# Kernel tuning notes

Hardware: AMD Instinct MI355X
Metric: run time of the kernel (lower is better)

## Reference

```python
import jax, jax.numpy as jnp
import numpy as np

N_STEPS = 8  # fixed-step RK4 over t in [0, 1]


def setup_inputs() -> dict:
    key = jax.random.key(0)
    ks = jax.random.split(key, 4)
    B, D, H = 512, 64, 512
    x = jax.random.normal(ks[0], (B, D), jnp.float32)
    # MLP vector field f(t, x): input = concat([x, t]) -> H -> H -> D
    W1 = jax.random.normal(ks[1], (D + 1, H), jnp.float32) / jnp.sqrt(D + 1.0)
    b1 = jnp.zeros((H,), jnp.float32)
    W2 = jax.random.normal(ks[2], (H, H), jnp.float32) / jnp.sqrt(float(H))
    b2 = jnp.zeros((H,), jnp.float32)
    W3 = jax.random.normal(ks[3], (H, D), jnp.float32) / jnp.sqrt(float(H))
    b3 = jnp.zeros((D,), jnp.float32)
    return {"x": x, "W1": W1, "b1": b1, "W2": W2, "b2": b2, "W3": W3, "b3": b3}


def reference(x, W1, b1, W2, b2, W3, b3):
    dt = 1.0 / N_STEPS

    def vf_single(t, xi):
        # xi: [D], t: scalar -> [D]
        h = jnp.concatenate([xi, t[None]])
        h = jnp.tanh(h @ W1 + b1)
        h = jnp.tanh(h @ W2 + b2)
        return h @ W3 + b3

    def aug_dyn(t, xb):
        # dx/dt = f(x, t);  d(log_det)/dt = -trace(df/dx)  (exact divergence)
        f_s = lambda xi: vf_single(t, xi)
        dx = jax.vmap(f_s)(xb)                      # [B, D]
        jac = jax.vmap(jax.jacfwd(f_s))(xb)         # [B, D, D]
        tr = jnp.trace(jac, axis1=-2, axis2=-1)     # [B]
        return dx, -tr

    def step(carry, i):
        xb, ld = carry
        t0 = i.astype(jnp.float32) * dt
        k1x, k1l = aug_dyn(t0, xb)
        k2x, k2l = aug_dyn(t0 + 0.5 * dt, xb + 0.5 * dt * k1x)
        k3x, k3l = aug_dyn(t0 + 0.5 * dt, xb + 0.5 * dt * k2x)
        k4x, k4l = aug_dyn(t0 + dt, xb + dt * k3x)
        xb = xb + (dt / 6.0) * (k1x + 2.0 * k2x + 2.0 * k3x + k4x)
        ld = ld + (dt / 6.0) * (k1l + 2.0 * k2l + 2.0 * k3l + k4l)
        return (xb, ld), None

    ld0 = jnp.zeros((x.shape[0],), x.dtype)
    (z, log_det), _ = jax.lax.scan(step, (x, ld0), jnp.arange(N_STEPS))
    return z, log_det
```

## Files before the change

kernel.cpp:

```cpp
#include <hip/hip_runtime.h>

#define NSTEPS 8
#define DT (1.0f / NSTEPS)

typedef __bf16 bfv8 __attribute__((ext_vector_type(8)));
typedef float f32x4 __attribute__((ext_vector_type(4)));

static __device__ __forceinline__ float fast_tanh(float x) {
  float e = __expf(2.f * x);
  return 1.f - 2.f * __builtin_amdgcn_rcpf(e + 1.f);
}

static __device__ __forceinline__ f32x4 splat4(float v) {
  f32x4 r; r[0] = v; r[1] = v; r[2] = v; r[3] = v; return r;
}

__global__ __launch_bounds__(256) void pre_kernel(
    const float* __restrict__ W1, const float* __restrict__ W2,
    const float* __restrict__ W3, __bf16* __restrict__ W1P,
    __bf16* __restrict__ W2P, __bf16* __restrict__ GtP,
    __bf16* __restrict__ W3P) {
  int t = blockIdx.x * 256 + threadIdx.x;
  if (t < 4096) {
    int kq = t >> 9, col = t & 511;
    bfv8 o;
#pragma unroll
    for (int e = 0; e < 8; ++e) o[e] = (__bf16)W1[(kq * 8 + e) * 512 + col];
    *(bfv8*)(W1P + t * 8) = o;
  } else if (t < 36864) {
    int g = t - 4096;
    int kc = g >> 9, col = g & 511;
    bfv8 o;
#pragma unroll
    for (int e = 0; e < 8; ++e) o[e] = (__bf16)W2[(kc * 8 + e) * 512 + col];
    *(bfv8*)(W2P + g * 8) = o;
  } else if (t < 69632) {
    int g = t - 36864;
    int kc = g >> 9, j = g & 511;
    float w1c[64];
#pragma unroll
    for (int m = 0; m < 64; ++m) w1c[m] = W1[m * 512 + j];
    bfv8 o;
#pragma unroll
    for (int e = 0; e < 8; ++e) {
      int k = kc * 8 + e;
      float s = 0.f;
#pragma unroll
      for (int m = 0; m < 64; ++m) s = fmaf(w1c[m], W3[k * 64 + m], s);
      o[e] = (__bf16)(s * W2[j * 512 + k]);
    }
    *(bfv8*)(GtP + g * 8) = o;
  } else if (t < 73728) {
    int g = t - 69632;
    int kc = g >> 6, m = g & 63;
    bfv8 o;
#pragma unroll
    for (int e = 0; e < 8; ++e) o[e] = (__bf16)W3[(kc * 8 + e) * 64 + m];
    *(bfv8*)(W3P + g * 8) = o;
  }
}

__global__ __launch_bounds__(512, 2) void cnf_kernel(
    const float* __restrict__ x, const float* __restrict__ b1,
    const float* __restrict__ W1, const float* __restrict__ b2,
    const float* __restrict__ b3, const __bf16* __restrict__ W1P,
    const __bf16* __restrict__ W2P, const __bf16* __restrict__ GtP,
    const __bf16* __restrict__ W3P, float* __restrict__ out) {
  __shared__ __bf16 h1s[8192];
  __shared__ __bf16 h2s[8192];
  __shared__ __bf16 vs[8192];
  __shared__ __bf16 xins[1024];
  __shared__ float kcur[1024];
  __shared__ float trbuf[16];

  const int tid = threadIdx.x;
  const int lane = tid & 63;
  const int w = tid >> 6;
  const int lr = lane & 15;
  const int lq = lane >> 4;
  const int rowbase = blockIdx.x * 16;
  const char* h1c = (const char*)h1s;
  const char* h2c = (const char*)h2s;
  const char* vsc = (const char*)vs;

  float b1c[4], w1tc[4], b2c[4], b3c[4];
#pragma unroll
  for (int n = 0; n < 4; ++n) {
    const int col = (w * 4 + n) * 16 + lr;
    b1c[n] = b1[col];
    w1tc[n] = W1[64 * 512 + col];
    b2c[n] = b2[col];
    b3c[n] = b3[n * 16 + lr];
  }

  float xbA = 0.f, xbB = 0.f, kaA = 0.f, kaB = 0.f, ldv = 0.f, ldacc = 0.f;

#pragma unroll 1
  for (int ev = 0; ev <= 4 * NSTEPS; ++ev) {
    const int g = ev & 3;
    {
      float xwA, xwB;
      if (ev == 0) {
        xbA = x[rowbase * 64 + tid];
        xbB = x[rowbase * 64 + 512 + tid];
        xwA = xbA; xwB = xbB;
        kcur[tid] = 0.f; kcur[tid + 512] = 0.f;
        if (tid < 16) trbuf[tid] = 0.f;
      } else {
        const int gp = (ev - 1) & 3;
        const float k0 = kcur[tid], k1 = kcur[tid + 512];
        kcur[tid] = 0.f; kcur[tid + 512] = 0.f;
        float tv = 0.f;
        if (tid < 16) { tv = trbuf[tid]; trbuf[tid] = 0.f; }
        if (gp < 3) {
          const float wg = (gp == 0) ? 1.f : 2.f;
          const float cn = (gp == 2) ? DT : 0.5f * DT;
          kaA += wg * k0; kaB += wg * k1;
          xwA = xbA + cn * k0; xwB = xbB + cn * k1;
          if (tid < 16) ldacc += wg * tv;
        } else {
          xbA += (DT / 6.f) * (kaA + k0);
          xbB += (DT / 6.f) * (kaB + k1);
          kaA = 0.f; kaB = 0.f;
          xwA = xbA; xwB = xbB;
          if (tid < 16) { ldv -= (DT / 6.f) * (ldacc + tv); ldacc = 0.f; }
        }
      }
      if (ev == 4 * NSTEPS) {
        out[rowbase * 64 + tid] = xwA;
        out[rowbase * 64 + 512 + tid] = xwB;
        if (tid < 16) out[512 * 64 + rowbase + tid] = ldv;
        break;
      }
      xins[tid] = (__bf16)xwA;
      xins[tid + 512] = (__bf16)xwB;
    }
    __syncthreads();

    {
      const float tval =
          (ev >> 2) * DT + ((g == 0) ? 0.f : (g == 3) ? DT : 0.5f * DT);
      const bfv8 a0 = *(const bfv8*)&xins[lr * 64 + lq * 8];
      const bfv8 a1 = *(const bfv8*)&xins[lr * 64 + 32 + lq * 8];
      bfv8 ring[4];
#pragma unroll
      for (int p = 0; p < 4; ++p)
        ring[p] = *(const bfv8*)(W1P + ((p & 1) * 4 + lq) * 4096 +
                                 ((w * 4 + (p >> 1)) * 16 + lr) * 8);
      f32x4 C = splat4(0.f);
#pragma unroll
      for (int f = 0; f < 8; ++f) {
        const int n = f >> 1, h = f & 1;
        if (h == 0) C = splat4(b1c[n] + tval * w1tc[n]);
        C = __builtin_amdgcn_mfma_f32_16x16x32_bf16(h ? a1 : a0, ring[f & 3],
                                                    C, 0, 0, 0);
        if (f < 4) {
          const int f4 = f + 4;
          ring[f & 3] = *(const bfv8*)(W1P + ((f4 & 1) * 4 + lq) * 4096 +
                                       ((w * 4 + (f4 >> 1)) * 16 + lr) * 8);
        }
        if (h == 1) {
#pragma unroll
          for (int r = 0; r < 4; ++r) {
            const int row = lq * 4 + r;
            const int col = (w * 4 + n) * 16 + lr;
            *(__bf16*)((char*)h1s + row * 1024 +
                       ((col * 2) ^ ((row & 7) << 4))) = (__bf16)fast_tanh(C[r]);
          }
        }
      }
    }
    __syncthreads();

    {
      bfv8 A[16];
#pragma unroll
      for (int c = 0; c < 16; ++c)
        A[c] = *(const bfv8*)(h1c + lr * 1024 +
                              (((c * 64) + lq * 16) ^ ((lr & 7) << 4)));
      bfv8 ring[4];
#pragma unroll
      for (int p = 0; p < 4; ++p)
        ring[p] = *(const bfv8*)(W2P + (p * 4 + lq) * 4096 +
                                 ((w * 4) * 16 + lr) * 8);
      f32x4 C = splat4(0.f);
#pragma unroll
      for (int f = 0; f < 64; ++f) {
        const int c = f & 15, t = f >> 4;
        if (c == 0) C = splat4(0.f);
        C = __builtin_amdgcn_mfma_f32_16x16x32_bf16(A[c], ring[f & 3], C, 0, 0,
                                                    0);
        if (f < 60) {
          const int f4 = f + 4;
          ring[f & 3] = *(const bfv8*)(W2P + ((f4 & 15) * 4 + lq) * 4096 +
                                       ((w * 4 + (f4 >> 4)) * 16 + lr) * 8);
        }
        if (c == 15) {
#pragma unroll
          for (int r = 0; r < 4; ++r) {
            const int row = lq * 4 + r;
            const int col = (w * 4 + t) * 16 + lr;
            const float tv = fast_tanh(C[r] + b2c[t]);
            const int bo = row * 1024 + ((col * 2) ^ ((row & 7) << 4));
            *(__bf16*)((char*)h2s + bo) = (__bf16)tv;
            *(__bf16*)((char*)vs + bo) = (__bf16)(1.f - tv * tv);
          }
        }
      }
    }
    __syncthreads();

    {
      bfv8 A[16];
#pragma unroll
      for (int c = 0; c < 16; ++c)
        A[c] = *(const bfv8*)(vsc + lr * 1024 +
                              (((c * 64) + lq * 16) ^ ((lr & 7) << 4)));
      bfv8 ring[4];
#pragma unroll
      for (int p = 0; p < 4; ++p)
        ring[p] = *(const bfv8*)(GtP + (p * 4 + lq) * 4096 +
                                 ((w * 4) * 16 + lr) * 8);
      f32x4 C = splat4(0.f);
      float pacc[4] = {0.f, 0.f, 0.f, 0.f};
#pragma unroll
      for (int f = 0; f < 64; ++f) {
        const int c = f & 15, t = f >> 4;
        if (c == 0) C = splat4(0.f);
        C = __builtin_amdgcn_mfma_f32_16x16x32_bf16(A[c], ring[f & 3], C, 0, 0,
                                                    0);
        if (f < 60) {
          const int f4 = f + 4;
          ring[f & 3] = *(const bfv8*)(GtP + ((f4 & 15) * 4 + lq) * 4096 +
                                       ((w * 4 + (f4 >> 4)) * 16 + lr) * 8);
        }
        if (c == 15) {
#pragma unroll
          for (int r = 0; r < 4; ++r) {
            const int row = lq * 4 + r;
            const int col = (w * 4 + t) * 16 + lr;
            const float h1v = (float)*(const __bf16*)(
                h1c + row * 1024 + ((col * 2) ^ ((row & 7) << 4)));
            pacc[r] += C[r] * (1.f - h1v * h1v);
          }
        }
      }
#pragma unroll
      for (int r = 0; r < 4; ++r) {
        float p = pacc[r];
        p += __shfl_xor(p, 1);
        p += __shfl_xor(p, 2);
        p += __shfl_xor(p, 4);
        p += __shfl_xor(p, 8);
        if (lr == 0) atomicAdd(&trbuf[lq * 4 + r], p);
      }
    }

    {
      bfv8 A2[2];
#pragma unroll
      for (int h = 0; h < 2; ++h)
        A2[h] = *(const bfv8*)(h2c + lr * 1024 +
                               (((w * 128 + h * 64 + lq * 16)) ^
                                ((lr & 7) << 4)));
      bfv8 ring[4];
#pragma unroll
      for (int p = 0; p < 4; ++p)
        ring[p] = *(const bfv8*)(W3P + (w * 8 + (p & 1) * 4 + lq) * 512 +
                                 ((p >> 1) * 16 + lr) * 8);
      f32x4 C = splat4(0.f);
#pragma unroll
      for (int f = 0; f < 8; ++f) {
        const int mt = f >> 1, h = f & 1;
        if (h == 0) C = splat4((w == 0) ? b3c[mt] : 0.f);
        C = __builtin_amdgcn_mfma_f32_16x16x32_bf16(A2[h], ring[f & 3], C, 0,
                                                    0, 0);
        if (f < 4) {
          const int f4 = f + 4;
          ring[f & 3] =
              *(const bfv8*)(W3P + (w * 8 + (f4 & 1) * 4 + lq) * 512 +
                             ((f4 >> 1) * 16 + lr) * 8);
        }
        if (h == 1) {
#pragma unroll
          for (int r = 0; r < 4; ++r)
            atomicAdd(&kcur[(lq * 4 + r) * 64 + mt * 16 + lr], C[r]);
        }
      }
    }
    __syncthreads();
  }
}

extern "C" void kernel_launch(void* const* d_in, const int* in_sizes, int n_in,
                              void* d_out, int out_size, void* d_ws,
                              size_t ws_size, hipStream_t stream) {
  const float* x = (const float*)d_in[0];
  const float* W1 = (const float*)d_in[1];
  const float* b1 = (const float*)d_in[2];
  const float* W2 = (const float*)d_in[3];
  const float* b2 = (const float*)d_in[4];
  const float* W3 = (const float*)d_in[5];
  const float* b3 = (const float*)d_in[6];
  float* out = (float*)d_out;
  __bf16* wsb = (__bf16*)d_ws;

  __bf16* W1P = wsb;
  __bf16* W2P = wsb + 32768;
  __bf16* GtP = wsb + 294912;
  __bf16* W3P = wsb + 557056;

  pre_kernel<<<288, 256, 0, stream>>>(W1, W2, W3, W1P, W2P, GtP, W3P);
  cnf_kernel<<<32, 512, 0, stream>>>(x, b1, W1, b2, b3, W1P, W2P, GtP, W3P,
                                     out);
}
```

Before: 1.085 ms.

## Stream weights through triple-buffered LDS ring via async global_load_lds

```diff
diff --git a/kernel.cpp b/kernel.cpp
--- a/kernel.cpp
+++ b/kernel.cpp
@@ -1,4 +1,5 @@
 #include <hip/hip_runtime.h>
+#include <stdint.h>
 
 #define NSTEPS 8
 #define DT (1.0f / NSTEPS)
@@ -10,9 +11,36 @@
   float e = __expf(2.f * x);
   return 1.f - 2.f * __builtin_amdgcn_rcpf(e + 1.f);
 }
-
 static __device__ __forceinline__ f32x4 splat4(float v) {
   f32x4 r; r[0] = v; r[1] = v; r[2] = v; r[3] = v; return r;
+}
+
+#define FENCE __builtin_amdgcn_sched_barrier(0)
+#define PIPEBAR()                                                  \
+  do {                                                             \
+    FENCE;                                                         \
+    asm volatile("s_waitcnt vmcnt(4) lgkmcnt(0)" ::: "memory");    \
+    __builtin_amdgcn_s_barrier();                                  \
+    FENCE;                                                         \
+  } while (0)
+#define ENDBAR()                                                   \
+  do {                                                             \
+    FENCE;                                                         \
+    asm volatile("s_waitcnt lgkmcnt(0)" ::: "memory");             \
+    __builtin_amdgcn_s_barrier();                                  \
+    FENCE;                                                         \
+  } while (0)
+
+static __device__ __forceinline__ void stage_chunk(const char* gsrc,
+                                                   char* ldst, int tid) {
+#pragma unroll
+  for (int i = 0; i < 4; ++i)
+    __builtin_amdgcn_global_load_lds(
+        (const __attribute__((address_space(1))) uint32_t*)(gsrc + i * 8192 +
+                                                            tid * 16),
+        (__attribute__((address_space(3))) uint32_t*)(ldst + i * 8192 +
+                                                      tid * 16),
+        16, 0, 0);
 }
 
 __global__ __launch_bounds__(256) void pre_kernel(
@@ -63,12 +91,11 @@
 __global__ __launch_bounds__(512, 2) void cnf_kernel(
     const float* __restrict__ x, const float* __restrict__ b1,
     const float* __restrict__ W1, const float* __restrict__ b2,
-    const float* __restrict__ b3, const __bf16* __restrict__ W1P,
-    const __bf16* __restrict__ W2P, const __bf16* __restrict__ GtP,
+    const float* __restrict__ b3, const char* __restrict__ stream,
     const __bf16* __restrict__ W3P, float* __restrict__ out) {
+  __shared__ char ring[3 * 32768];
   __shared__ __bf16 h1s[8192];
   __shared__ __bf16 h2s[8192];
-  __shared__ __bf16 vs[8192];
   __shared__ __bf16 xins[1024];
   __shared__ float kcur[1024];
   __shared__ float trbuf[16];
@@ -81,7 +108,6 @@
   const int rowbase = blockIdx.x * 16;
   const char* h1c = (const char*)h1s;
   const char* h2c = (const char*)h2s;
-  const char* vsc = (const char*)vs;
 
   float b1c[4], w1tc[4], b2c[4], b3c[4];
 #pragma unroll
@@ -93,11 +119,24 @@
     b3c[n] = b3[n * 16 + lr];
   }
 
+  const int bbase = lq * 8192 + w * 1024 + lr * 16;
+
   float xbA = 0.f, xbB = 0.f, kaA = 0.f, kaB = 0.f, ldv = 0.f, ldacc = 0.f;
+
+  int sc = 0;
+  stage_chunk(stream, ring, tid);
+  stage_chunk(stream + 32768, ring + 32768, tid);
+
+#define STEP_HEAD(T_NEXT)                                                \
+  do {                                                                   \
+    PIPEBAR();                                                           \
+    int ss_ = sc + 2; if (ss_ >= 3) ss_ -= 3;                            \
+    stage_chunk(stream + (T_NEXT) * 32768, ring + ss_ * 32768, tid);     \
+  } while (0)
+#define STEP_TAIL() do { sc = (sc + 1 == 3) ? 0 : sc + 1; } while (0)
 
 #pragma unroll 1
   for (int ev = 0; ev <= 4 * NSTEPS; ++ev) {
-    const int g = ev & 3;
     {
       float xwA, xwB;
       if (ev == 0) {
@@ -135,125 +174,115 @@
       xins[tid] = (__bf16)xwA;
       xins[tid + 512] = (__bf16)xwB;
     }
-    __syncthreads();
+
+    const int g = ev & 3;
+    const float tval =
+        (ev >> 2) * DT + ((g == 0) ? 0.f : (g == 3) ? DT : 0.5f * DT);
+    f32x4 C[4];
 
     {
-      const float tval =
-          (ev >> 2) * DT + ((g == 0) ? 0.f : (g == 3) ? DT : 0.5f * DT);
+      STEP_HEAD(2);
       const bfv8 a0 = *(const bfv8*)&xins[lr * 64 + lq * 8];
+      const char* bs = ring + sc * 32768 + bbase;
+#pragma unroll
+      for (int n = 0; n < 4; ++n) {
+        C[n] = splat4(b1c[n] + tval * w1tc[n]);
+        C[n] = __builtin_amdgcn_mfma_f32_16x16x32_bf16(
+            a0, *(const bfv8*)(bs + n * 256), C[n], 0, 0, 0);
+      }
+      STEP_TAIL();
+    }
+    {
+      STEP_HEAD(3);
       const bfv8 a1 = *(const bfv8*)&xins[lr * 64 + 32 + lq * 8];
-      bfv8 ring[4];
-#pragma unroll
-      for (int p = 0; p < 4; ++p)
-        ring[p] = *(const bfv8*)(W1P + ((p & 1) * 4 + lq) * 4096 +
-                                 ((w * 4 + (p >> 1)) * 16 + lr) * 8);
-      f32x4 C = splat4(0.f);
-#pragma unroll
-      for (int f = 0; f < 8; ++f) {
-        const int n = f >> 1, h = f & 1;
-        if (h == 0) C = splat4(b1c[n] + tval * w1tc[n]);
-        C = __builtin_amdgcn_mfma_f32_16x16x32_bf16(h ? a1 : a0, ring[f & 3],
-                                                    C, 0, 0, 0);
-        if (f < 4) {
-          const int f4 = f + 4;
-          ring[f & 3] = *(const bfv8*)(W1P + ((f4 & 1) * 4 + lq) * 4096 +
-                                       ((w * 4 + (f4 >> 1)) * 16 + lr) * 8);
+      const char* bs = ring + sc * 32768 + bbase;
+#pragma unroll
+      for (int n = 0; n < 4; ++n) {
+        C[n] = __builtin_amdgcn_mfma_f32_16x16x32_bf16(
+            a1, *(const bfv8*)(bs + n * 256), C[n], 0, 0, 0);
+#pragma unroll
+        for (int r = 0; r < 4; ++r) {
+          const int row = lq * 4 + r;
+          const int col = (w * 4 + n) * 16 + lr;
+          *(__bf16*)((char*)h1s + row * 1024 + ((col * 2) ^ ((row & 7) << 4))) =
+              (__bf16)fast_tanh(C[n][r]);
         }
-        if (h == 1) {
+      }
+      STEP_TAIL();
+    }
+
+#pragma unroll
+    for (int c = 0; c < 16; ++c) {
+      STEP_HEAD(c + 4);
+      if (c == 0) {
+#pragma unroll
+        for (int n = 0; n < 4; ++n) C[n] = splat4(0.f);
+      }
+      const bfv8 A = *(const bfv8*)(h1c + lr * 1024 +
+                                    (((c * 64) + lq * 16) ^ ((lr & 7) << 4)));
+      const char* bs = ring + sc * 32768 + bbase;
+#pragma unroll
+      for (int n = 0; n < 4; ++n)
+        C[n] = __builtin_amdgcn_mfma_f32_16x16x32_bf16(
+            A, *(const bfv8*)(bs + n * 256), C[n], 0, 0, 0);
+      if (c == 15) {
+#pragma unroll
+        for (int n = 0; n < 4; ++n)
 #pragma unroll
           for (int r = 0; r < 4; ++r) {
             const int row = lq * 4 + r;
             const int col = (w * 4 + n) * 16 + lr;
-            *(__bf16*)((char*)h1s + row * 1024 +
-                       ((col * 2) ^ ((row & 7) << 4))) = (__bf16)fast_tanh(C[r]);
+            const float tv = fast_tanh(C[n][r] + b2c[n]);
+            *(__bf16*)((char*)h2s + row * 1024 +
+                       ((col * 2) ^ ((row & 7) << 4))) = (__bf16)tv;
           }
-        }
-      }
-    }
-    __syncthreads();
-
-    {
-      bfv8 A[16];
-#pragma unroll
-      for (int c = 0; c < 16; ++c)
-        A[c] = *(const bfv8*)(h1c + lr * 1024 +
-                              (((c * 64) + lq * 16) ^ ((lr & 7) << 4)));
-      bfv8 ring[4];
-#pragma unroll
-      for (int p = 0; p < 4; ++p)
-        ring[p] = *(const bfv8*)(W2P + (p * 4 + lq) * 4096 +
-                                 ((w * 4) * 16 + lr) * 8);
-      f32x4 C = splat4(0.f);
-#pragma unroll
-      for (int f = 0; f < 64; ++f) {
-        const int c = f & 15, t = f >> 4;
-        if (c == 0) C = splat4(0.f);
-        C = __builtin_amdgcn_mfma_f32_16x16x32_bf16(A[c], ring[f & 3], C, 0, 0,
-                                                    0);
-        if (f < 60) {
-          const int f4 = f + 4;
-          ring[f & 3] = *(const bfv8*)(W2P + ((f4 & 15) * 4 + lq) * 4096 +
-                                       ((w * 4 + (f4 >> 4)) * 16 + lr) * 8);
-        }
-        if (c == 15) {
+      }
+      STEP_TAIL();
+    }
+
+#pragma unroll
+    for (int c = 0; c < 16; ++c) {
+      STEP_HEAD((c < 14) ? 20 + c : c - 14);
+      if (c == 0) {
+#pragma unroll
+        for (int n = 0; n < 4; ++n) C[n] = splat4(0.f);
+      }
+      const bfv8 hv = *(const bfv8*)(h2c + lr * 1024 +
+                                     (((c * 64) + lq * 16) ^ ((lr & 7) << 4)));
+      bfv8 av;
+#pragma unroll
+      for (int e = 0; e < 8; ++e) {
+        const float tv = (float)hv[e];
+        av[e] = (__bf16)(1.f - tv * tv);
+      }
+      const char* bs = ring + sc * 32768 + bbase;
+#pragma unroll
+      for (int n = 0; n < 4; ++n)
+        C[n] = __builtin_amdgcn_mfma_f32_16x16x32_bf16(
+            av, *(const bfv8*)(bs + n * 256), C[n], 0, 0, 0);
+      if (c == 15) {
+        float pacc[4] = {0.f, 0.f, 0.f, 0.f};
+#pragma unroll
+        for (int n = 0; n < 4; ++n)
 #pragma unroll
           for (int r = 0; r < 4; ++r) {
             const int row = lq * 4 + r;
-            const int col = (w * 4 + t) * 16 + lr;
-            const float tv = fast_tanh(C[r] + b2c[t]);
-            const int bo = row * 1024 + ((col * 2) ^ ((row & 7) << 4));
-            *(__bf16*)((char*)h2s + bo) = (__bf16)tv;
-            *(__bf16*)((char*)vs + bo) = (__bf16)(1.f - tv * tv);
-          }
-        }
-      }
-    }
-    __syncthreads();
-
-    {
-      bfv8 A[16];
-#pragma unroll
-      for (int c = 0; c < 16; ++c)
-        A[c] = *(const bfv8*)(vsc + lr * 1024 +
-                              (((c * 64) + lq * 16) ^ ((lr & 7) << 4)));
-      bfv8 ring[4];
-#pragma unroll
-      for (int p = 0; p < 4; ++p)
-        ring[p] = *(const bfv8*)(GtP + (p * 4 + lq) * 4096 +
-                                 ((w * 4) * 16 + lr) * 8);
-      f32x4 C = splat4(0.f);
-      float pacc[4] = {0.f, 0.f, 0.f, 0.f};
-#pragma unroll
-      for (int f = 0; f < 64; ++f) {
-        const int c = f & 15, t = f >> 4;
-        if (c == 0) C = splat4(0.f);
-        C = __builtin_amdgcn_mfma_f32_16x16x32_bf16(A[c], ring[f & 3], C, 0, 0,
-                                                    0);
-        if (f < 60) {
-          const int f4 = f + 4;
-          ring[f & 3] = *(const bfv8*)(GtP + ((f4 & 15) * 4 + lq) * 4096 +
-                                       ((w * 4 + (f4 >> 4)) * 16 + lr) * 8);
-        }
-        if (c == 15) {
-#pragma unroll
-          for (int r = 0; r < 4; ++r) {
-            const int row = lq * 4 + r;
-            const int col = (w * 4 + t) * 16 + lr;
+            const int col = (w * 4 + n) * 16 + lr;
             const float h1v = (float)*(const __bf16*)(
                 h1c + row * 1024 + ((col * 2) ^ ((row & 7) << 4)));
-            pacc[r] += C[r] * (1.f - h1v * h1v);
+            pacc[r] += C[n][r] * (1.f - h1v * h1v);
           }
+#pragma unroll
+        for (int r = 0; r < 4; ++r) {
+          float p = pacc[r];
+          p += __shfl_xor(p, 1);
+          p += __shfl_xor(p, 2);
+          p += __shfl_xor(p, 4);
+          p += __shfl_xor(p, 8);
+          if (lr == 0) atomicAdd(&trbuf[lq * 4 + r], p);
         }
       }
-#pragma unroll
-      for (int r = 0; r < 4; ++r) {
-        float p = pacc[r];
-        p += __shfl_xor(p, 1);
-        p += __shfl_xor(p, 2);
-        p += __shfl_xor(p, 4);
-        p += __shfl_xor(p, 8);
-        if (lr == 0) atomicAdd(&trbuf[lq * 4 + r], p);
-      }
+      STEP_TAIL();
     }
 
     {
@@ -261,34 +290,24 @@
 #pragma unroll
       for (int h = 0; h < 2; ++h)
         A2[h] = *(const bfv8*)(h2c + lr * 1024 +
-                               (((w * 128 + h * 64 + lq * 16)) ^
+                               ((w * 128 + h * 64 + lq * 16) ^
                                 ((lr & 7) << 4)));
-      bfv8 ring[4];
-#pragma unroll
-      for (int p = 0; p < 4; ++p)
-        ring[p] = *(const bfv8*)(W3P + (w * 8 + (p & 1) * 4 + lq) * 512 +
-                                 ((p >> 1) * 16 + lr) * 8);
-      f32x4 C = splat4(0.f);
+      f32x4 C3;
 #pragma unroll
       for (int f = 0; f < 8; ++f) {
         const int mt = f >> 1, h = f & 1;
-        if (h == 0) C = splat4((w == 0) ? b3c[mt] : 0.f);
-        C = __builtin_amdgcn_mfma_f32_16x16x32_bf16(A2[h], ring[f & 3], C, 0,
-                                                    0, 0);
-        if (f < 4) {
-          const int f4 = f + 4;
-          ring[f & 3] =
-              *(const bfv8*)(W3P + (w * 8 + (f4 & 1) * 4 + lq) * 512 +
-                             ((f4 >> 1) * 16 + lr) * 8);
+        if (h == 0) C3 = splat4((w == 0) ? b3c[mt] : 0.f);
+        const bfv8 B = *(const bfv8*)(W3P + (w * 8 + h * 4 + lq) * 512 +
+                                      (mt * 16 + lr) * 8);
+        C3 = __builtin_amdgcn_mfma_f32_16x16x32_bf16(A2[h], B, C3, 0, 0, 0);
+        if (h == 1) {
+#pragma unroll
+          for (int r = 0; r < 4; ++r)
+            atomicAdd(&kcur[(lq * 4 + r) * 64 + mt * 16 + lr], C3[r]);
         }
-        if (h == 1) {
-#pragma unroll
-          for (int r = 0; r < 4; ++r)
-            atomicAdd(&kcur[(lq * 4 + r) * 64 + mt * 16 + lr], C[r]);
-        }
-      }
-    }
-    __syncthreads();
+      }
+    }
+    ENDBAR();
   }
 }
 
@@ -311,6 +330,6 @@
   __bf16* W3P = wsb + 557056;
 
   pre_kernel<<<288, 256, 0, stream>>>(W1, W2, W3, W1P, W2P, GtP, W3P);
-  cnf_kernel<<<32, 512, 0, stream>>>(x, b1, W1, b2, b3, W1P, W2P, GtP, W3P,
+  cnf_kernel<<<32, 512, 0, stream>>>(x, b1, W1, b2, b3, (const char*)wsb, W3P,
                                      out);
 }
```

New measurement: 1.202 ms. 1.11x slower.

## Split hidden dimension across 8 blocks per row group with LDS-resident weights and inter-block sync

Applied to the files above, without the earlier changes.

```diff
diff --git a/kernel.cpp b/kernel.cpp
--- a/kernel.cpp
+++ b/kernel.cpp
@@ -1,295 +1,312 @@
 #include <hip/hip_runtime.h>
+#include <stdint.h>
 
 #define NSTEPS 8
 #define DT (1.0f / NSTEPS)
 
 typedef __bf16 bfv8 __attribute__((ext_vector_type(8)));
+typedef __bf16 bfv4 __attribute__((ext_vector_type(4)));
 typedef float f32x4 __attribute__((ext_vector_type(4)));
 
 static __device__ __forceinline__ float fast_tanh(float x) {
   float e = __expf(2.f * x);
   return 1.f - 2.f * __builtin_amdgcn_rcpf(e + 1.f);
 }
-
 static __device__ __forceinline__ f32x4 splat4(float v) {
   f32x4 r; r[0] = v; r[1] = v; r[2] = v; r[3] = v; return r;
 }
 
 __global__ __launch_bounds__(256) void pre_kernel(
     const float* __restrict__ W1, const float* __restrict__ W2,
-    const float* __restrict__ W3, __bf16* __restrict__ W1P,
-    __bf16* __restrict__ W2P, __bf16* __restrict__ GtP,
-    __bf16* __restrict__ W3P) {
+    const float* __restrict__ W3, __bf16* __restrict__ blob,
+    unsigned int* __restrict__ syncc) {
   int t = blockIdx.x * 256 + threadIdx.x;
+  if (t < 49152) syncc[t] = 0u;
+  if (t >= 73728) return;
+  bfv8 o;
+  int di;
   if (t < 4096) {
-    int kq = t >> 9, col = t & 511;
-    bfv8 o;
-#pragma unroll
-    for (int e = 0; e < 8; ++e) o[e] = (__bf16)W1[(kq * 8 + e) * 512 + col];
-    *(bfv8*)(W1P + t * 8) = o;
+    int kq = t >> 9, colg = t & 511;
+    int s = colg >> 6, c = colg & 63;
+    int f = kq >> 2, gg = (kq & 3) ^ ((c >> 1) & 3);
+    di = s * 73728 + f * 2048 + c * 32 + gg * 8;
+#pragma unroll
+    for (int e = 0; e < 8; ++e) o[e] = (__bf16)W1[(kq * 8 + e) * 512 + colg];
   } else if (t < 36864) {
-    int g = t - 4096;
-    int kc = g >> 9, col = g & 511;
-    bfv8 o;
-#pragma unroll
-    for (int e = 0; e < 8; ++e) o[e] = (__bf16)W2[(kc * 8 + e) * 512 + col];
-    *(bfv8*)(W2P + g * 8) = o;
+    int u = t - 4096;
+    int colg = u & 511, kc = u >> 9;
+    int s = colg >> 6, c = colg & 63;
+    int f = kc >> 2, gg = (kc & 3) ^ ((c >> 1) & 3);
+    di = s * 73728 + 4096 + f * 2048 + c * 32 + gg * 8;
+#pragma unroll
+    for (int e = 0; e < 8; ++e) o[e] = (__bf16)W2[(kc * 8 + e) * 512 + colg];
   } else if (t < 69632) {
-    int g = t - 36864;
-    int kc = g >> 9, j = g & 511;
+    int u = t - 36864;
+    int jg = u & 511, kc = u >> 9;
     float w1c[64];
 #pragma unroll
-    for (int m = 0; m < 64; ++m) w1c[m] = W1[m * 512 + j];
-    bfv8 o;
+    for (int m = 0; m < 64; ++m) w1c[m] = W1[m * 512 + jg];
+    int s = jg >> 6, c = jg & 63;
+    int f = kc >> 2, gg = (kc & 3) ^ ((c >> 1) & 3);
+    di = s * 73728 + 36864 + f * 2048 + c * 32 + gg * 8;
 #pragma unroll
     for (int e = 0; e < 8; ++e) {
       int k = kc * 8 + e;
-      float s = 0.f;
-#pragma unroll
-      for (int m = 0; m < 64; ++m) s = fmaf(w1c[m], W3[k * 64 + m], s);
-      o[e] = (__bf16)(s * W2[j * 512 + k]);
-    }
-    *(bfv8*)(GtP + g * 8) = o;
-  } else if (t < 73728) {
-    int g = t - 69632;
-    int kc = g >> 6, m = g & 63;
-    bfv8 o;
+      float sm = 0.f;
+#pragma unroll
+      for (int m = 0; m < 64; ++m) sm = fmaf(w1c[m], W3[k * 64 + m], sm);
+      o[e] = (__bf16)(sm * W2[jg * 512 + k]);
+    }
+  } else {
+    int u = t - 69632;
+    int m = u & 63, kc = u >> 6;
+    int tile = m >> 4, cm = m & 15;
+    int b = tile * 2 + (kc >> 5);
+    int f = (kc >> 2) & 7, gg = (kc & 3) ^ ((cm >> 1) & 3);
+    di = b * 73728 + 69632 + f * 512 + cm * 32 + gg * 8;
 #pragma unroll
     for (int e = 0; e < 8; ++e) o[e] = (__bf16)W3[(kc * 8 + e) * 64 + m];
-    *(bfv8*)(W3P + g * 8) = o;
   }
-}
-
-__global__ __launch_bounds__(512, 2) void cnf_kernel(
+  *(bfv8*)(blob + di) = o;
+}
+
+static __device__ __forceinline__ void gsync(unsigned int* cnt, int tid) {
+  __threadfence();
+  __syncthreads();
+  if (tid == 0) {
+    __hip_atomic_fetch_add(cnt, 1u, __ATOMIC_RELEASE, __HIP_MEMORY_SCOPE_AGENT);
+    int guard = 0;
+    while (__hip_atomic_load(cnt, __ATOMIC_RELAXED, __HIP_MEMORY_SCOPE_AGENT) <
+           8u) {
+      __builtin_amdgcn_s_sleep(2);
+      if (++guard > (1 << 22)) break;
+    }
+    (void)__hip_atomic_load(cnt, __ATOMIC_ACQUIRE, __HIP_MEMORY_SCOPE_AGENT);
+  }
+  __syncthreads();
+  __threadfence();
+}
+
+__global__ __launch_bounds__(256, 1) void cnf_kernel(
     const float* __restrict__ x, const float* __restrict__ b1,
-    const float* __restrict__ W1, const float* __restrict__ b2,
-    const float* __restrict__ b3, const __bf16* __restrict__ W1P,
-    const __bf16* __restrict__ W2P, const __bf16* __restrict__ GtP,
-    const __bf16* __restrict__ W3P, float* __restrict__ out) {
-  __shared__ __bf16 h1s[8192];
-  __shared__ __bf16 h2s[8192];
-  __shared__ __bf16 vs[8192];
-  __shared__ __bf16 xins[1024];
-  __shared__ float kcur[1024];
-  __shared__ float trbuf[16];
+    const float* __restrict__ W1f, const float* __restrict__ b2,
+    const float* __restrict__ b3, const __bf16* __restrict__ blob,
+    char* __restrict__ actg, unsigned int* __restrict__ syncc,
+    float* __restrict__ out) {
+  __shared__ char wlds[147456];
+  __shared__ char actv[8192];
+  __shared__ char xins[2048];
+  __shared__ float kxl[256];
+  __shared__ float trl[16];
 
   const int tid = threadIdx.x;
   const int lane = tid & 63;
   const int w = tid >> 6;
   const int lr = lane & 15;
   const int lq = lane >> 4;
-  const int rowbase = blockIdx.x * 16;
-  const char* h1c = (const char*)h1s;
-  const char* h2c = (const char*)h2s;
-  const char* vsc = (const char*)vs;
-
-  float b1c[4], w1tc[4], b2c[4], b3c[4];
-#pragma unroll
-  for (int n = 0; n < 4; ++n) {
-    const int col = (w * 4 + n) * 16 + lr;
-    b1c[n] = b1[col];
-    w1tc[n] = W1[64 * 512 + col];
-    b2c[n] = b2[col];
-    b3c[n] = b3[n * 16 + lr];
+  const int g = blockIdx.x & 31;
+  const int b = blockIdx.x >> 5;
+  const int rowbase = g * 16;
+
+  {
+    const char* src = (const char*)blob + (size_t)b * 147456;
+#pragma unroll 1
+    for (int i = 0; i < 36; ++i) {
+      const int off = (w * 36 + i) * 1024 + lane * 16;
+      __builtin_amdgcn_global_load_lds(
+          (const __attribute__((address_space(1))) uint32_t*)(src + off),
+          (__attribute__((address_space(3))) uint32_t*)(wlds + off), 16, 0, 0);
+    }
   }
 
-  float xbA = 0.f, xbB = 0.f, kaA = 0.f, kaB = 0.f, ldv = 0.f, ldacc = 0.f;
+  const int colg = b * 64 + w * 16 + lr;
+  const float b1c = b1[colg];
+  const float w1tc = W1f[64 * 512 + colg];
+  const float b2c = b2[colg];
+  const float b3v = ((b & 1) == 0) ? b3[(b >> 1) * 16 + (tid & 15)] : 0.f;
+  const int gx = lq ^ ((lr >> 1) & 3);
+  const int bcol = (w * 16 + lr) * 64 + gx * 16;
+
+  char* gb = actg + (size_t)g * 65536;
+  __bf16* h1buf = (__bf16*)gb;
+  __bf16* h2buf = (__bf16*)(gb + 16384);
+  __bf16* vbuf = (__bf16*)(gb + 32768);
+  float* kxbuf = (float*)(gb + 49152);
+  float* trbufg = (float*)(gb + 57344);
+  unsigned int* scg = syncc + g * 96 * 16;
+
+  asm volatile("s_waitcnt vmcnt(0)" ::: "memory");
+  __syncthreads();
+
+  const int srow = tid >> 4, scol = (tid & 15) * 4;
+  float xb[4], ka[4];
+  float ldv = 0.f, ldacc = 0.f;
+
+#define MFMA(A, Boff, C)                                                      \
+  C = __builtin_amdgcn_mfma_f32_16x16x32_bf16(                                \
+      A, *(const bfv8*)(wlds + (Boff)), C, 0, 0, 0)
+#define AFRAG(c)                                                              \
+  (*(const bfv8*)(actv + lr * 512 + ((((c) * 64) + lq * 16) ^ ((lr & 7) << 4))))
+#define STAGE_ACT(SRCBUF, HF)                                                 \
+  do {                                                                        \
+    const int row_ = tid >> 4, ch_ = tid & 15;                                \
+    bfv8 d0_ = *(const bfv8*)((SRCBUF) + row_ * 512 + (HF) * 256 + ch_ * 8);  \
+    bfv8 d1_ =                                                                \
+        *(const bfv8*)((SRCBUF) + row_ * 512 + (HF) * 256 + 128 + ch_ * 8);   \
+    __syncthreads();                                                          \
+    *(bfv8*)(actv + row_ * 512 + ((ch_ * 16) ^ ((row_ & 7) << 4))) = d0_;     \
+    *(bfv8*)(actv + row_ * 512 + ((ch_ * 16 + 256) ^ ((row_ & 7) << 4))) =    \
+        d1_;                                                                  \
+    __syncthreads();                                                          \
+  } while (0)
 
 #pragma unroll 1
   for (int ev = 0; ev <= 4 * NSTEPS; ++ev) {
-    const int g = ev & 3;
-    {
-      float xwA, xwB;
-      if (ev == 0) {
-        xbA = x[rowbase * 64 + tid];
-        xbB = x[rowbase * 64 + 512 + tid];
-        xwA = xbA; xwB = xbB;
-        kcur[tid] = 0.f; kcur[tid + 512] = 0.f;
-        if (tid < 16) trbuf[tid] = 0.f;
+    float xw[4];
+    if (ev == 0) {
+      const float* xr = x + (rowbase + srow) * 64 + scol;
+#pragma unroll
+      for (int i = 0; i < 4; ++i) { xb[i] = xr[i]; ka[i] = 0.f; xw[i] = xb[i]; }
+    } else {
+      const int gp = (ev - 1) & 3;
+      const int tt = scol >> 4, cb2 = scol & 15;
+      float kv[4];
+#pragma unroll
+      for (int i = 0; i < 4; ++i)
+        kv[i] = kxbuf[(tt * 2) * 256 + srow * 16 + cb2 + i] +
+                kxbuf[(tt * 2 + 1) * 256 + srow * 16 + cb2 + i];
+      float tv = 0.f;
+      if (tid < 16) {
+#pragma unroll
+        for (int bb = 0; bb < 8; ++bb) tv += trbufg[bb * 16 + tid];
+      }
+      if (gp < 3) {
+        const float wg = (gp == 0) ? 1.f : 2.f;
+        const float cn = (gp == 2) ? DT : 0.5f * DT;
+#pragma unroll
+        for (int i = 0; i < 4; ++i) {
+          ka[i] += wg * kv[i];
+          xw[i] = xb[i] + cn * kv[i];
+        }
+        if (tid < 16) ldacc += wg * tv;
       } else {
-        const int gp = (ev - 1) & 3;
-        const float k0 = kcur[tid], k1 = kcur[tid + 512];
-        kcur[tid] = 0.f; kcur[tid + 512] = 0.f;
-        float tv = 0.f;
-        if (tid < 16) { tv = trbuf[tid]; trbuf[tid] = 0.f; }
-        if (gp < 3) {
-          const float wg = (gp == 0) ? 1.f : 2.f;
-          const float cn = (gp == 2) ? DT : 0.5f * DT;
-          kaA += wg * k0; kaB += wg * k1;
-          xwA = xbA + cn * k0; xwB = xbB + cn * k1;
-          if (tid < 16) ldacc += wg * tv;
-        } else {
-          xbA += (DT / 6.f) * (kaA + k0);
-          xbB += (DT / 6.f) * (kaB + k1);
-          kaA = 0.f; kaB = 0.f;
-          xwA = xbA; xwB = xbB;
-          if (tid < 16) { ldv -= (DT / 6.f) * (ldacc + tv); ldacc = 0.f; }
+#pragma unroll
+        for (int i = 0; i < 4; ++i) {
+          xb[i] += (DT / 6.f) * (ka[i] + kv[i]);
+          ka[i] = 0.f;
+          xw[i] = xb[i];
         }
-      }
-      if (ev == 4 * NSTEPS) {
-        out[rowbase * 64 + tid] = xwA;
-        out[rowbase * 64 + 512 + tid] = xwB;
+        if (tid < 16) { ldv -= (DT / 6.f) * (ldacc + tv); ldacc = 0.f; }
+      }
+    }
+    if (ev == 4 * NSTEPS) {
+      if (b == 0) {
+        float* orow = out + (rowbase + srow) * 64 + scol;
+#pragma unroll
+        for (int i = 0; i < 4; ++i) orow[i] = xw[i];
         if (tid < 16) out[512 * 64 + rowbase + tid] = ldv;
-        break;
-      }
-      xins[tid] = (__bf16)xwA;
-      xins[tid + 512] = (__bf16)xwB;
+      }
+      break;
+    }
+    {
+      bfv4 pk;
+#pragma unroll
+      for (int i = 0; i < 4; ++i) pk[i] = (__bf16)xw[i];
+      *(bfv4*)(xins + srow * 128 + ((scol * 2) ^ ((srow & 7) << 4))) = pk;
     }
     __syncthreads();
 
-    {
-      const float tval =
-          (ev >> 2) * DT + ((g == 0) ? 0.f : (g == 3) ? DT : 0.5f * DT);
-      const bfv8 a0 = *(const bfv8*)&xins[lr * 64 + lq * 8];
-      const bfv8 a1 = *(const bfv8*)&xins[lr * 64 + 32 + lq * 8];
-      bfv8 ring[4];
-#pragma unroll
-      for (int p = 0; p < 4; ++p)
-        ring[p] = *(const bfv8*)(W1P + ((p & 1) * 4 + lq) * 4096 +
-                                 ((w * 4 + (p >> 1)) * 16 + lr) * 8);
-      f32x4 C = splat4(0.f);
-#pragma unroll
-      for (int f = 0; f < 8; ++f) {
-        const int n = f >> 1, h = f & 1;
-        if (h == 0) C = splat4(b1c[n] + tval * w1tc[n]);
-        C = __builtin_amdgcn_mfma_f32_16x16x32_bf16(h ? a1 : a0, ring[f & 3],
-                                                    C, 0, 0, 0);
-        if (f < 4) {
-          const int f4 = f + 4;
-          ring[f & 3] = *(const bfv8*)(W1P + ((f4 & 1) * 4 + lq) * 4096 +
-                                       ((w * 4 + (f4 >> 1)) * 16 + lr) * 8);
+    const int gq = ev & 3;
+    const float tval =
+        (ev >> 2) * DT + ((gq == 0) ? 0.f : (gq == 3) ? DT : 0.5f * DT);
+    float ureg[4];
+    {
+      bfv8 a0 = *(const bfv8*)(xins + lr * 128 + ((lq * 16) ^ ((lr & 7) << 4)));
+      bfv8 a1 =
+          *(const bfv8*)(xins + lr * 128 + ((64 + lq * 16) ^ ((lr & 7) << 4)));
+      f32x4 C = splat4(b1c + tval * w1tc);
+      MFMA(a0, 0 * 4096 + bcol, C);
+      MFMA(a1, 1 * 4096 + bcol, C);
+#pragma unroll
+      for (int r = 0; r < 4; ++r) {
+        const float t1 = fast_tanh(C[r]);
+        ureg[r] = 1.f - t1 * t1;
+        h1buf[(lq * 4 + r) * 512 + colg] = (__bf16)t1;
+      }
+    }
+    gsync(scg + (ev * 3 + 0) * 16, tid);
+
+    {
+      f32x4 Ca = splat4(0.f), Cb = splat4(0.f);
+#pragma unroll
+      for (int hf = 0; hf < 2; ++hf) {
+        STAGE_ACT(h1buf, hf);
+#pragma unroll
+        for (int c2 = 0; c2 < 4; ++c2) {
+          const int c = c2 * 2, f = hf * 8 + c;
+          bfv8 A0 = AFRAG(c), A1 = AFRAG(c + 1);
+          MFMA(A0, 8192 + f * 4096 + bcol, Ca);
+          MFMA(A1, 8192 + (f + 1) * 4096 + bcol, Cb);
         }
-        if (h == 1) {
-#pragma unroll
-          for (int r = 0; r < 4; ++r) {
-            const int row = lq * 4 + r;
-            const int col = (w * 4 + n) * 16 + lr;
-            *(__bf16*)((char*)h1s + row * 1024 +
-                       ((col * 2) ^ ((row & 7) << 4))) = (__bf16)fast_tanh(C[r]);
-          }
+      }
+#pragma unroll
+      for (int r = 0; r < 4; ++r) {
+        const float t2 = fast_tanh(Ca[r] + Cb[r] + b2c);
+        h2buf[(lq * 4 + r) * 512 + colg] = (__bf16)t2;
+        vbuf[(lq * 4 + r) * 512 + colg] = (__bf16)(1.f - t2 * t2);
+      }
+    }
+    if (tid < 16) trl[tid] = 0.f;
+    kxl[tid] = b3v;
+    gsync(scg + (ev * 3 + 1) * 16, tid);
+
+    {
+      f32x4 Ca = splat4(0.f), Cb = splat4(0.f);
+#pragma unroll
+      for (int hf = 0; hf < 2; ++hf) {
+        STAGE_ACT(vbuf, hf);
+#pragma unroll
+        for (int c2 = 0; c2 < 4; ++c2) {
+          const int c = c2 * 2, f = hf * 8 + c;
+          bfv8 A0 = AFRAG(c), A1 = AFRAG(c + 1);
+          MFMA(A0, 73728 + f * 4096 + bcol, Ca);
+          MFMA(A1, 73728 + (f + 1) * 4096 + bcol, Cb);
         }
       }
+      float pacc[4];
+#pragma unroll
+      for (int r = 0; r < 4; ++r) pacc[r] = (Ca[r] + Cb[r]) * ureg[r];
+#pragma unroll
+      for (int r = 0; r < 4; ++r) {
+        pacc[r] += __shfl_xor(pacc[r], 1);
+        pacc[r] += __shfl_xor(pacc[r], 2);
+        pacc[r] += __shfl_xor(pacc[r], 4);
+        pacc[r] += __shfl_xor(pacc[r], 8);
+      }
+      if (lr == 0) {
+#pragma unroll
+        for (int r = 0; r < 4; ++r) atomicAdd(&trl[lq * 4 + r], pacc[r]);
+      }
+    }
+
+    {
+      STAGE_ACT(h2buf, b & 1);
+      f32x4 C3 = splat4(0.f);
+      bfv8 A0 = AFRAG(2 * w), A1 = AFRAG(2 * w + 1);
+      MFMA(A0, 139264 + (2 * w) * 1024 + lr * 64 + gx * 16, C3);
+      MFMA(A1, 139264 + (2 * w + 1) * 1024 + lr * 64 + gx * 16, C3);
+#pragma unroll
+      for (int r = 0; r < 4; ++r)
+        atomicAdd(&kxl[(lq * 4 + r) * 16 + lr], C3[r]);
     }
     __syncthreads();
-
-    {
-      bfv8 A[16];
-#pragma unroll
-      for (int c = 0; c < 16; ++c)
-        A[c] = *(const bfv8*)(h1c + lr * 1024 +
-                              (((c * 64) + lq * 16) ^ ((lr & 7) << 4)));
-      bfv8 ring[4];
-#pragma unroll
-      for (int p = 0; p < 4; ++p)
-        ring[p] = *(const bfv8*)(W2P + (p * 4 + lq) * 4096 +
-                                 ((w * 4) * 16 + lr) * 8);
-      f32x4 C = splat4(0.f);
-#pragma unroll
-      for (int f = 0; f < 64; ++f) {
-        const int c = f & 15, t = f >> 4;
-        if (c == 0) C = splat4(0.f);
-        C = __builtin_amdgcn_mfma_f32_16x16x32_bf16(A[c], ring[f & 3], C, 0, 0,
-                                                    0);
-        if (f < 60) {
-          const int f4 = f + 4;
-          ring[f & 3] = *(const bfv8*)(W2P + ((f4 & 15) * 4 + lq) * 4096 +
-                                       ((w * 4 + (f4 >> 4)) * 16 + lr) * 8);
-        }
-        if (c == 15) {
-#pragma unroll
-          for (int r = 0; r < 4; ++r) {
-            const int row = lq * 4 + r;
-            const int col = (w * 4 + t) * 16 + lr;
-            const float tv = fast_tanh(C[r] + b2c[t]);
-            const int bo = row * 1024 + ((col * 2) ^ ((row & 7) << 4));
-            *(__bf16*)((char*)h2s + bo) = (__bf16)tv;
-            *(__bf16*)((char*)vs + bo) = (__bf16)(1.f - tv * tv);
-          }
-        }
-      }
-    }
-    __syncthreads();
-
-    {
-      bfv8 A[16];
-#pragma unroll
-      for (int c = 0; c < 16; ++c)
-        A[c] = *(const bfv8*)(vsc + lr * 1024 +
-                              (((c * 64) + lq * 16) ^ ((lr & 7) << 4)));
-      bfv8 ring[4];
-#pragma unroll
-      for (int p = 0; p < 4; ++p)
-        ring[p] = *(const bfv8*)(GtP + (p * 4 + lq) * 4096 +
-                                 ((w * 4) * 16 + lr) * 8);
-      f32x4 C = splat4(0.f);
-      float pacc[4] = {0.f, 0.f, 0.f, 0.f};
-#pragma unroll
-      for (int f = 0; f < 64; ++f) {
-        const int c = f & 15, t = f >> 4;
-        if (c == 0) C = splat4(0.f);
-        C = __builtin_amdgcn_mfma_f32_16x16x32_bf16(A[c], ring[f & 3], C, 0, 0,
-                                                    0);
-        if (f < 60) {
-          const int f4 = f + 4;
-          ring[f & 3] = *(const bfv8*)(GtP + ((f4 & 15) * 4 + lq) * 4096 +
-                                       ((w * 4 + (f4 >> 4)) * 16 + lr) * 8);
-        }
-        if (c == 15) {
-#pragma unroll
-          for (int r = 0; r < 4; ++r) {
-            const int row = lq * 4 + r;
-            const int col = (w * 4 + t) * 16 + lr;
-            const float h1v = (float)*(const __bf16*)(
-                h1c + row * 1024 + ((col * 2) ^ ((row & 7) << 4)));
-            pacc[r] += C[r] * (1.f - h1v * h1v);
-          }
-        }
-      }
-#pragma unroll
-      for (int r = 0; r < 4; ++r) {
-        float p = pacc[r];
-        p += __shfl_xor(p, 1);
-        p += __shfl_xor(p, 2);
-        p += __shfl_xor(p, 4);
-        p += __shfl_xor(p, 8);
-        if (lr == 0) atomicAdd(&trbuf[lq * 4 + r], p);
-      }
-    }
-
-    {
-      bfv8 A2[2];
-#pragma unroll
-      for (int h = 0; h < 2; ++h)
-        A2[h] = *(const bfv8*)(h2c + lr * 1024 +
-                               (((w * 128 + h * 64 + lq * 16)) ^
-                                ((lr & 7) << 4)));
-      bfv8 ring[4];
-#pragma unroll
-      for (int p = 0; p < 4; ++p)
-        ring[p] = *(const bfv8*)(W3P + (w * 8 + (p & 1) * 4 + lq) * 512 +
-                                 ((p >> 1) * 16 + lr) * 8);
-      f32x4 C = splat4(0.f);
-#pragma unroll
-      for (int f = 0; f < 8; ++f) {
-        const int mt = f >> 1, h = f & 1;
-        if (h == 0) C = splat4((w == 0) ? b3c[mt] : 0.f);
-        C = __builtin_amdgcn_mfma_f32_16x16x32_bf16(A2[h], ring[f & 3], C, 0,
-                                                    0, 0);
-        if (f < 4) {
-          const int f4 = f + 4;
-          ring[f & 3] =
-              *(const bfv8*)(W3P + (w * 8 + (f4 & 1) * 4 + lq) * 512 +
-                             ((f4 >> 1) * 16 + lr) * 8);
-        }
-        if (h == 1) {
-#pragma unroll
-          for (int r = 0; r < 4; ++r)
-            atomicAdd(&kcur[(lq * 4 + r) * 64 + mt * 16 + lr], C[r]);
-        }
-      }
-    }
-    __syncthreads();
+    kxbuf[b * 256 + tid] = kxl[tid];
+    if (tid < 16) trbufg[b * 16 + tid] = trl[tid];
+    gsync(scg + (ev * 3 + 2) * 16, tid);
   }
+#undef MFMA
+#undef AFRAG
+#undef STAGE_ACT
 }
 
 extern "C" void kernel_launch(void* const* d_in, const int* in_sizes, int n_in,
@@ -303,14 +320,12 @@
   const float* W3 = (const float*)d_in[5];
   const float* b3 = (const float*)d_in[6];
   float* out = (float*)d_out;
-  __bf16* wsb = (__bf16*)d_ws;
-
-  __bf16* W1P = wsb;
-  __bf16* W2P = wsb + 32768;
-  __bf16* GtP = wsb + 294912;
-  __bf16* W3P = wsb + 557056;
-
-  pre_kernel<<<288, 256, 0, stream>>>(W1, W2, W3, W1P, W2P, GtP, W3P);
-  cnf_kernel<<<32, 512, 0, stream>>>(x, b1, W1, b2, b3, W1P, W2P, GtP, W3P,
-                                     out);
-}
+
+  __bf16* blob = (__bf16*)d_ws;
+  unsigned int* syncc = (unsigned int*)((char*)d_ws + 2097152);
+  char* actg = (char*)d_ws + 4194304;
+
+  pre_kernel<<<288, 256, 0, stream>>>(W1, W2, W3, blob, syncc);
+  cnf_kernel<<<256, 256, 0, stream>>>(x, b1, W1, b2, b3, blob, actg, syncc,
+                                      out);
+}
```

New measurement: 3.952 ms. 3.64x slower.

## Deepen weight prefetch ring, stagger K order per block, stream A fragments from LDS

Applied to the files above, without the earlier changes.

```diff
diff --git a/kernel.cpp b/kernel.cpp
--- a/kernel.cpp
+++ b/kernel.cpp
@@ -79,6 +79,7 @@
   const int lr = lane & 15;
   const int lq = lane >> 4;
   const int rowbase = blockIdx.x * 16;
+  const int rot = (3 * blockIdx.x + (blockIdx.x >> 3)) & 15;
   const char* h1c = (const char*)h1s;
   const char* h2c = (const char*)h2s;
   const char* vsc = (const char*)vs;
@@ -173,27 +174,28 @@
     __syncthreads();
 
     {
-      bfv8 A[16];
-#pragma unroll
-      for (int c = 0; c < 16; ++c)
-        A[c] = *(const bfv8*)(h1c + lr * 1024 +
-                              (((c * 64) + lq * 16) ^ ((lr & 7) << 4)));
-      bfv8 ring[4];
-#pragma unroll
-      for (int p = 0; p < 4; ++p)
-        ring[p] = *(const bfv8*)(W2P + (p * 4 + lq) * 4096 +
+      bfv8 ring[8];
+#pragma unroll
+      for (int p = 0; p < 8; ++p) {
+        const int cp = (p + rot) & 15;
+        ring[p] = *(const bfv8*)(W2P + (cp * 4 + lq) * 4096 +
                                  ((w * 4) * 16 + lr) * 8);
+      }
       f32x4 C = splat4(0.f);
 #pragma unroll
       for (int f = 0; f < 64; ++f) {
         const int c = f & 15, t = f >> 4;
         if (c == 0) C = splat4(0.f);
-        C = __builtin_amdgcn_mfma_f32_16x16x32_bf16(A[c], ring[f & 3], C, 0, 0,
-                                                    0);
-        if (f < 60) {
-          const int f4 = f + 4;
-          ring[f & 3] = *(const bfv8*)(W2P + ((f4 & 15) * 4 + lq) * 4096 +
-                                       ((w * 4 + (f4 >> 4)) * 16 + lr) * 8);
+        const int cp = (c + rot) & 15;
+        const bfv8 A = *(const bfv8*)(
+            h1c + lr * 1024 + (((cp * 64) + lq * 16) ^ ((lr & 7) << 4)));
+        C = __builtin_amdgcn_mfma_f32_16x16x32_bf16(A, ring[f & 7], C, 0, 0, 0);
+        if (f < 56) {
+          const int f8 = f + 8;
+          const int cp8 = ((f8 & 15) + rot) & 15;
+          ring[f & 7] =
+              *(const bfv8*)(W2P + (cp8 * 4 + lq) * 4096 +
+                             ((w * 4 + (f8 >> 4)) * 16 + lr) * 8);
         }
         if (c == 15) {
 #pragma unroll
@@ -211,28 +213,29 @@
     __syncthreads();
 
     {
-      bfv8 A[16];
-#pragma unroll
-      for (int c = 0; c < 16; ++c)
-        A[c] = *(const bfv8*)(vsc + lr * 1024 +
-                              (((c * 64) + lq * 16) ^ ((lr & 7) << 4)));
-      bfv8 ring[4];
-#pragma unroll
-      for (int p = 0; p < 4; ++p)
-        ring[p] = *(const bfv8*)(GtP + (p * 4 + lq) * 4096 +
+      bfv8 ring[8];
+#pragma unroll
+      for (int p = 0; p < 8; ++p) {
+        const int cp = (p + rot) & 15;
+        ring[p] = *(const bfv8*)(GtP + (cp * 4 + lq) * 4096 +
                                  ((w * 4) * 16 + lr) * 8);
+      }
       f32x4 C = splat4(0.f);
       float pacc[4] = {0.f, 0.f, 0.f, 0.f};
 #pragma unroll
       for (int f = 0; f < 64; ++f) {
         const int c = f & 15, t = f >> 4;
         if (c == 0) C = splat4(0.f);
-        C = __builtin_amdgcn_mfma_f32_16x16x32_bf16(A[c], ring[f & 3], C, 0, 0,
-                                                    0);
-        if (f < 60) {
-          const int f4 = f + 4;
-          ring[f & 3] = *(const bfv8*)(GtP + ((f4 & 15) * 4 + lq) * 4096 +
-                                       ((w * 4 + (f4 >> 4)) * 16 + lr) * 8);
+        const int cp = (c + rot) & 15;
+        const bfv8 A = *(const bfv8*)(
+            vsc + lr * 1024 + (((cp * 64) + lq * 16) ^ ((lr & 7) << 4)));
+        C = __builtin_amdgcn_mfma_f32_16x16x32_bf16(A, ring[f & 7], C, 0, 0, 0);
+        if (f < 56) {
+          const int f8 = f + 8;
+          const int cp8 = ((f8 & 15) + rot) & 15;
+          ring[f & 7] =
+              *(const bfv8*)(GtP + (cp8 * 4 + lq) * 4096 +
+                             ((w * 4 + (f8 >> 4)) * 16 + lr) * 8);
         }
         if (c == 15) {
 #pragma unroll
```

New measurement: 1.124 ms. 1.04x slower.
